# Kernel tuning notes

Hardware: AMD Instinct MI355X
Metric: run time of the kernel (lower is better)

Reference implementation:

```python
import jax, jax.numpy as jnp
import numpy as np

L = 2            # layer_num
NNEI = 120       # neighbors
ED = 64          # embed_dim
HD = 128         # hidden_dim
B = 4096         # nframes * nloc
SCALING = HD ** (-0.5)
LN_EPS = 1e-5


def _l2norm(x):
    # torch F.normalize: x / max(||x||, 1e-12)
    n = jnp.sqrt(jnp.sum(x * x, axis=-1, keepdims=True))
    return x / jnp.maximum(n, 1e-12)


def setup_inputs() -> dict:
    key = jax.random.key(0)
    ks = jax.random.split(key, 10)
    input_G = jax.random.normal(ks[0], (B, NNEI, ED), dtype=jnp.float32)
    nei_mask = jax.random.randint(ks[1], (B, NNEI), 0, 2) > 0
    nei_mask = nei_mask.at[:, 0].set(True)  # ensure >=1 valid neighbor (avoid all -inf rows)
    r = jax.random.normal(ks[2], (B, NNEI, 3), dtype=jnp.float32)
    input_r = _l2norm(r)  # normalized radial
    std_in = 1.0 / np.sqrt(3 * HD + ED)
    std_out = 1.0 / np.sqrt(ED + HD)
    in_w = jax.random.normal(ks[3], (L, ED, 3 * HD), dtype=jnp.float32) * std_in
    in_b = jax.random.normal(ks[4], (L, 3 * HD), dtype=jnp.float32)
    out_w = jax.random.normal(ks[5], (L, HD, ED), dtype=jnp.float32) * std_out
    out_b = jax.random.normal(ks[6], (L, ED), dtype=jnp.float32)
    ln_g = jnp.ones((L, ED), dtype=jnp.float32)
    ln_b = jnp.zeros((L, ED), dtype=jnp.float32)
    return {"input_G": input_G, "nei_mask": nei_mask, "input_r": input_r,
            "in_w": in_w, "in_b": in_b, "out_w": out_w, "out_b": out_b,
            "ln_g": ln_g, "ln_b": ln_b}


def _layer_norm(x, g, b):
    mu = jnp.mean(x, axis=-1, keepdims=True)
    var = jnp.mean((x - mu) ** 2, axis=-1, keepdims=True)
    return (x - mu) * jax.lax.rsqrt(var + LN_EPS) * g + b


def reference(input_G, nei_mask, input_r, in_w, in_b, out_w, out_b, ln_g, ln_b):
    # angular gate: [B, nnei, nnei]
    ang = jnp.einsum('bnd,bmd->bnm', input_r, input_r)
    mask_k = nei_mask[:, None, :]   # mask over keys
    mask_q = nei_mask[:, :, None]   # mask over queries
    x = input_G
    for l in range(L):
        residual = x
        qkv = jnp.einsum('bne,ef->bnf', x, in_w[l]) + in_b[l]
        q, k, v = jnp.split(qkv, 3, axis=-1)           # each [B, nnei, HD]
        q = _l2norm(q) * SCALING
        k = _l2norm(k)
        v = _l2norm(v)
        aw = jnp.einsum('bnh,bmh->bnm', q, k)
        aw = jnp.where(mask_k, aw, -jnp.inf)
        aw = jax.nn.softmax(aw, axis=-1)
        aw = jnp.where(mask_q, aw, 0.0)
        aw = aw * ang                                   # dotr angular gating
        o = jnp.einsum('bnm,bmh->bnh', aw, v)
        x = residual + jnp.einsum('bnh,he->bne', o, out_w[l]) + out_b[l]
        x = _layer_norm(x, ln_g[l], ln_b[l])            # post_ln
    return x
```

## Files before the change

kernel.cpp:

```cpp
#include <hip/hip_runtime.h>
#include <math.h>

#define LAYERS 2
#define NNEI 120
#define NPAD 128
#define ED 64
#define HD 128
#define NB 4096
#define F3 (3*HD)
#define SCALING 0.088388347648318447f
#define LN_EPS 1e-5f
#define T 1024
#define XP 72
#define QPAD 136

typedef unsigned short u16;
typedef unsigned int u32;
typedef unsigned char u8;
typedef float f32x4 __attribute__((ext_vector_type(4)));
typedef short bf16x8 __attribute__((ext_vector_type(8)));

__device__ __forceinline__ float bf2f(u16 u) { return __uint_as_float(((u32)u) << 16); }
__device__ __forceinline__ u16 f2bf(float f) {
  __bf16 b = (__bf16)f;
  return __builtin_bit_cast(u16, b);
}
__device__ __forceinline__ u32 pk2bf(float lo, float hi) {
  return (u32)f2bf(lo) | ((u32)f2bf(hi) << 16);
}
__device__ __forceinline__ float gldr(const void* p, long i, bool f32) {
  return f32 ? ((const float*)p)[i] : bf2f(((const u16*)p)[i]);
}
__device__ __forceinline__ float red16sum(float v) {
  v += __shfl_xor(v, 1); v += __shfl_xor(v, 2);
  v += __shfl_xor(v, 4); v += __shfl_xor(v, 8);
  return v;
}

#define MFMA(a, b, d) (d) = __builtin_amdgcn_mfma_f32_16x16x32_bf16((a), (b), (d), 0, 0, 0)

__device__ __forceinline__ void gload_lds16(const u16* src, u16* dst) {
  __builtin_amdgcn_global_load_lds(
      (const __attribute__((address_space(1))) u32*)(const void*)src,
      (__attribute__((address_space(3))) u32*)(void*)dst, 16, 0, 0);
}

__device__ __forceinline__ void stage16(const u16* __restrict__ hi, const u16* __restrict__ lo,
                                        long base, int kstride, u16* sbuf, int wave, int lane) {
  const int col = 4 * wave + (lane >> 4);
  const int slot = lane & 15;
  const int chunk = (slot & 7) ^ (col & 7);
  const u16* src = ((slot < 8) ? hi : lo) + base + (long)col * kstride + 8 * chunk;
  gload_lds16(src, sbuf + wave * 512);
}

__device__ __forceinline__ bf16x8 rdfrag(const u16* sbuf, int col, int chunk, int c7, int lo) {
  const int slot = (chunk ^ c7) + (lo << 3);
  return *(const bf16x8*)(sbuf + col * 128 + slot * 8);
}

__global__ void detect_kernel(const u16* __restrict__ G,
                              const u8* __restrict__ mask,
                              int* __restrict__ flags) {
  __shared__ int sf[2];
  const int t = threadIdx.x;
  if (t < 2) sf[t] = 0;
  __syncthreads();
  int isf = 0;
  for (int i = t; i < 256; i += 256) {
    int e = (G[2 * i] >> 7) & 0xff;
    if (e >= 150) isf = 1;
  }
  int mb = 0;
  for (int i = t; i < 4096; i += 256) {
    if (i && (i & 3) && mask[i]) mb = 1;
  }
  if (isf) atomicOr(&sf[0], 1);
  if (mb) atomicOr(&sf[1], 1);
  __syncthreads();
  if (t < 2) flags[t] = sf[t];
}

__global__ void prep_kernel(const void* __restrict__ in_w, const void* __restrict__ out_w,
                            u16* __restrict__ wt_hi, u16* __restrict__ wt_lo,
                            u16* __restrict__ ow_hi, u16* __restrict__ ow_lo,
                            const int* __restrict__ flags) {
  const bool f32 = flags[0] != 0;
  const int i = blockIdx.x * blockDim.x + threadIdx.x;
  if (i < LAYERS * F3 * ED) {
    const int l = i / (F3 * ED);
    const int rem = i % (F3 * ED);
    const int f = rem / ED;
    const int e = rem % ED;
    const long src = (long)(l * ED + e) * F3 + f;
    const float w = f32 ? ((const float*)in_w)[src] : bf2f(((const u16*)in_w)[src]);
    const u16 h = f2bf(w);
    wt_hi[i] = h;
    wt_lo[i] = f2bf(w - bf2f(h));
  }
  if (i < LAYERS * ED * HD) {
    const int l = i / (ED * HD);
    const int rem = i % (ED * HD);
    const int e = rem / HD;
    const int hh = rem % HD;
    const long src = (long)(l * HD + hh) * ED + e;
    const float w = f32 ? ((const float*)out_w)[src] : bf2f(((const u16*)out_w)[src]);
    const u16 h = f2bf(w);
    ow_hi[i] = h;
    ow_lo[i] = f2bf(w - bf2f(h));
  }
}

__global__ __launch_bounds__(T) void nwa_kernel(
    const void* __restrict__ G, const void* __restrict__ mask,
    const void* __restrict__ rr,
    const void* __restrict__ in_b, const void* __restrict__ out_b,
    const void* __restrict__ ln_g, const void* __restrict__ ln_b,
    const u16* __restrict__ wt_hi, const u16* __restrict__ wt_lo,
    const u16* __restrict__ ow_hi, const u16* __restrict__ ow_lo,
    void* __restrict__ out, const int* __restrict__ flags)
{
  const bool f32f = flags[0] != 0;
  const bool mbyte = flags[1] != 0;

  __shared__ __align__(16) u16 x_hi[NPAD][XP];
  __shared__ __align__(16) u16 x_lo[NPAD][XP];
  __shared__ __align__(16) u16 q_s[NPAD][QPAD];
  __shared__ __align__(16) u16 k_s[NPAD][QPAD];
  __shared__ __align__(16) u16 vT_s[HD][QPAD];
  __shared__ __align__(16) float r_s[NPAD][4];
  __shared__ __align__(16) float pA[2][8][16];
  __shared__ __align__(16) float pB[2][8][16];
  __shared__ int m_s[NPAD];

  const int b = blockIdx.x;
  const int t = threadIdx.x;
  const int wave = t >> 6;
  const int band = wave & 7;
  const int half = wave >> 3;
  const int lane = t & 63;
  const int g = lane >> 4;
  const int c = lane & 15;
  const int c7 = c & 7;
  u16* sbase = &q_s[0][0];

  {
    const long gbase = (long)b * (NNEI * ED);
    for (int i = t; i < NNEI * ED; i += T) {
      const int rrow = i >> 6, cc = i & 63;
      if (f32f) {
        const float v = ((const float*)G)[gbase + i];
        const u16 h = f2bf(v);
        x_hi[rrow][cc] = h;
        x_lo[rrow][cc] = f2bf(v - bf2f(h));
      } else {
        x_hi[rrow][cc] = ((const u16*)G)[gbase + i];
        x_lo[rrow][cc] = 0;
      }
    }
    for (int i = t; i < (NPAD - NNEI) * ED; i += T) {
      x_hi[NNEI + (i >> 6)][i & 63] = 0;
      x_lo[NNEI + (i >> 6)][i & 63] = 0;
    }
    const long rbase = (long)b * (NNEI * 3);
    const long mbase = (long)b * NNEI;
    for (int i = t; i < NPAD; i += T) {
      if (i < NNEI) {
        r_s[i][0] = gldr(rr, rbase + i * 3 + 0, f32f);
        r_s[i][1] = gldr(rr, rbase + i * 3 + 1, f32f);
        r_s[i][2] = gldr(rr, rbase + i * 3 + 2, f32f);
        r_s[i][3] = 0.f;
        m_s[i] = mbyte ? (int)((const u8*)mask)[mbase + i] : ((const int*)mask)[mbase + i];
      } else {
        r_s[i][0] = 0.f; r_s[i][1] = 0.f; r_s[i][2] = 0.f; r_s[i][3] = 0.f;
        m_s[i] = 0;
      }
    }
  }
  stage16(wt_hi, wt_lo, (long)2 * 4096, 64, sbase, wave, lane);
  __syncthreads();

  int vm[4];
  #pragma unroll
  for (int mtl = 0; mtl < 4; ++mtl) vm[mtl] = m_s[16 * (4 * half + mtl) + c];
  float qmr[4];
  #pragma unroll
  for (int r = 0; r < 4; ++r) qmr[r] = m_s[16 * band + 4 * g + r] ? 1.f : 0.f;

  for (int l = 0; l < LAYERS; ++l) {
    const long wofs = (long)l * (F3 * ED);
    const long bbase = (long)l * F3;
    const long oofs = (long)l * (ED * HD);
    const bool use_lo = f32f || (l > 0);

    bf16x8 a_hi[2], a_lo[2];
    #pragma unroll
    for (int kf = 0; kf < 2; ++kf) {
      a_hi[kf] = *(const bf16x8*)&x_hi[16 * band + c][32 * kf + 8 * g];
      a_lo[kf] = *(const bf16x8*)&x_lo[16 * band + c][32 * kf + 8 * g];
    }
    f32x4 accQ[4], accB[4];
    #pragma unroll
    for (int j = 0; j < 4; ++j) { accQ[j] = (f32x4){0,0,0,0}; accB[j] = (f32x4){0,0,0,0}; }

    #pragma unroll
    for (int ss = 0; ss < 6; ++ss) {
      const int n = (ss + 2) % 6;
      if (ss < 5)
        stage16(wt_hi, wt_lo, wofs + (long)((ss + 3) % 6) * 4096, 64,
                sbase + ((ss + 1) & 1) * 8192, wave, lane);
      if (ss == 2) {
        const f32x4 sa = *(const f32x4*)&pA[0][band][4 * g];
        const f32x4 sb4 = *(const f32x4*)&pA[1][band][4 * g];
        float invr[4];
        #pragma unroll
        for (int r = 0; r < 4; ++r) invr[r] = rsqrtf(fmaxf(sa[r] + sb4[r], 1e-24f));
        #pragma unroll
        for (int j = 0; j < 4; ++j) {
          const int nt = 4 * (j >> 1) + 2 * half + (j & 1);
          #pragma unroll
          for (int r = 0; r < 4; ++r)
            k_s[16 * band + 4 * g + r][16 * nt + c] = f2bf(accB[j][r] * invr[r]);
          accB[j] = (f32x4){0,0,0,0};
        }
      }
      if (ss == 4) {
        const f32x4 sa = *(const f32x4*)&pB[0][band][4 * g];
        const f32x4 sb4 = *(const f32x4*)&pB[1][band][4 * g];
        float invr[4];
        #pragma unroll
        for (int r = 0; r < 4; ++r) invr[r] = rsqrtf(fmaxf(sa[r] + sb4[r], 1e-24f));
        #pragma unroll
        for (int j = 0; j < 4; ++j) {
          const int nt = 4 * (j >> 1) + 2 * half + (j & 1);
          const u32 p01 = pk2bf(accB[j][0] * invr[0], accB[j][1] * invr[1]);
          const u32 p23 = pk2bf(accB[j][2] * invr[2], accB[j][3] * invr[3]);
          *(u32*)&vT_s[16 * nt + c][16 * band + 4 * g + 0] = p01;
          *(u32*)&vT_s[16 * nt + c][16 * band + 4 * g + 2] = p23;
        }
      }
      const u16* sb = sbase + (ss & 1) * 8192;
      #pragma unroll
      for (int ctl = 0; ctl < 2; ++ctl) {
        const int col = 16 * (2 * half + ctl) + c;
        const int j = 2 * (n & 1) + ctl;
        const bf16x8 bh0 = rdfrag(sb, col, g, c7, 0);
        const bf16x8 bh1 = rdfrag(sb, col, 4 + g, c7, 0);
        const bf16x8 bl0 = rdfrag(sb, col, g, c7, 1);
        const bf16x8 bl1 = rdfrag(sb, col, 4 + g, c7, 1);
        f32x4 d = (n < 2) ? accQ[j] : accB[j];
        MFMA(a_hi[0], bh0, d); MFMA(a_hi[1], bh1, d);
        if (use_lo) { MFMA(a_lo[0], bh0, d); MFMA(a_lo[1], bh1, d); }
        MFMA(a_hi[0], bl0, d); MFMA(a_hi[1], bl1, d);
        if (n < 2) accQ[j] = d; else accB[j] = d;
      }
      if (ss == 1 || ss == 3 || ss == 5) {
        const int fo = (ss == 1) ? 128 : (ss == 3) ? 256 : 0;
        f32x4* acc = (ss == 5) ? accQ : accB;
        #pragma unroll
        for (int j = 0; j < 4; ++j) {
          const int nt = 4 * (j >> 1) + 2 * half + (j & 1);
          const float bias = gldr(in_b, bbase + fo + 16 * nt + c, f32f);
          acc[j][0] += bias; acc[j][1] += bias; acc[j][2] += bias; acc[j][3] += bias;
        }
        float* dst = (ss == 3) ? &pB[half][band][0] : &pA[half][band][0];
        #pragma unroll
        for (int r = 0; r < 4; ++r) {
          const float ssum = acc[0][r] * acc[0][r] + acc[1][r] * acc[1][r] +
                             acc[2][r] * acc[2][r] + acc[3][r] * acc[3][r];
          const float red = red16sum(ssum);
          if (c == 0) dst[4 * g + r] = red;
        }
      }
      __syncthreads();
    }
    {
      const f32x4 sa = *(const f32x4*)&pA[0][band][4 * g];
      const f32x4 sb4 = *(const f32x4*)&pA[1][band][4 * g];
      float invr[4];
      #pragma unroll
      for (int r = 0; r < 4; ++r) invr[r] = SCALING * rsqrtf(fmaxf(sa[r] + sb4[r], 1e-24f));
      #pragma unroll
      for (int j = 0; j < 4; ++j) {
        const int nt = 4 * (j >> 1) + 2 * half + (j & 1);
        #pragma unroll
        for (int r = 0; r < 4; ++r)
          q_s[16 * band + 4 * g + r][16 * nt + c] = f2bf(accQ[j][r] * invr[r]);
      }
    }
    __syncthreads();

    f32x4 s4[4];
    {
      bf16x8 aq[4];
      #pragma unroll
      for (int kf = 0; kf < 4; ++kf)
        aq[kf] = *(const bf16x8*)&q_s[16 * band + c][32 * kf + 8 * g];
      #pragma unroll
      for (int mtl = 0; mtl < 4; ++mtl) {
        const u16* kp = &k_s[16 * (4 * half + mtl) + c][8 * g];
        f32x4 d = {0.f, 0.f, 0.f, 0.f};
        #pragma unroll
        for (int kf = 0; kf < 4; ++kf)
          MFMA(aq[kf], *(const bf16x8*)(kp + 32 * kf), d);
        s4[mtl] = d;
      }
    }
    {
      float psum[4] = {0.f, 0.f, 0.f, 0.f};
      #pragma unroll
      for (int mtl = 0; mtl < 4; ++mtl) {
        #pragma unroll
        for (int r = 0; r < 4; ++r) {
          const float e = vm[mtl] ? __expf(s4[mtl][r]) : 0.f;
          s4[mtl][r] = e;
          psum[r] += e;
        }
      }
      #pragma unroll
      for (int r = 0; r < 4; ++r) {
        const float red = red16sum(psum[r]);
        if (c == 0) pA[half][band][4 * g + r] = red;
      }
    }
    __syncthreads();
    {
      const f32x4 sa = *(const f32x4*)&pA[0][band][4 * g];
      const f32x4 sb4 = *(const f32x4*)&pA[1][band][4 * g];
      float inv[4];
      f32x4 rn[4];
      #pragma unroll
      for (int r = 0; r < 4; ++r) {
        inv[r] = qmr[r] / (sa[r] + sb4[r]);
        rn[r] = *(const f32x4*)&r_s[16 * band + 4 * g + r][0];
      }
      #pragma unroll
      for (int mtl = 0; mtl < 4; ++mtl) {
        const int mt = 4 * half + mtl;
        const f32x4 rm = *(const f32x4*)&r_s[16 * mt + c][0];
        #pragma unroll
        for (int r = 0; r < 4; ++r) {
          const float w = s4[mtl][r] * inv[r] *
              (rn[r][0] * rm[0] + rn[r][1] * rm[1] + rn[r][2] * rm[2]);
          q_s[16 * band + 4 * g + r][16 * mt + c] = f2bf(w);
        }
      }
    }
    __syncthreads();

    {
      bf16x8 pa[4];
      #pragma unroll
      for (int kf = 0; kf < 4; ++kf)
        pa[kf] = *(const bf16x8*)&q_s[16 * band + c][32 * kf + 8 * g];
      f32x4 o4[4];
      #pragma unroll
      for (int htl = 0; htl < 4; ++htl) {
        const u16* vp = &vT_s[16 * (4 * half + htl) + c][8 * g];
        f32x4 d = {0.f, 0.f, 0.f, 0.f};
        #pragma unroll
        for (int kf = 0; kf < 4; ++kf)
          MFMA(pa[kf], *(const bf16x8*)(vp + 32 * kf), d);
        o4[htl] = d;
      }
      #pragma unroll
      for (int htl = 0; htl < 4; ++htl)
        #pragma unroll
        for (int r = 0; r < 4; ++r)
          k_s[16 * band + 4 * g + r][16 * (4 * half + htl) + c] = f2bf(o4[htl][r]);
    }
    __syncthreads();

    bf16x8 ao[4];
    #pragma unroll
    for (int kf = 0; kf < 4; ++kf)
      ao[kf] = *(const bf16x8*)&k_s[16 * band + c][32 * kf + 8 * g];
    stage16(ow_hi, ow_lo, oofs, 128, sbase, wave, lane);
    __syncthreads();
    f32x4 dv[2];
    dv[0] = (f32x4){0,0,0,0}; dv[1] = (f32x4){0,0,0,0};
    #pragma unroll
    for (int kh = 0; kh < 2; ++kh) {
      if (kh == 0) stage16(ow_hi, ow_lo, oofs + 64, 128, sbase + 8192, wave, lane);
      const u16* sb = sbase + kh * 8192;
      #pragma unroll
      for (int ntl = 0; ntl < 2; ++ntl) {
        const int col = 16 * (2 * half + ntl) + c;
        #pragma unroll
        for (int kfl = 0; kfl < 2; ++kfl) {
          const bf16x8 bh = rdfrag(sb, col, 4 * kfl + g, c7, 0);
          const bf16x8 bl = rdfrag(sb, col, 4 * kfl + g, c7, 1);
          MFMA(ao[2 * kh + kfl], bh, dv[ntl]);
          MFMA(ao[2 * kh + kfl], bl, dv[ntl]);
        }
      }
      if (kh == 0) __syncthreads();
    }
    if (l + 1 < LAYERS)
      stage16(wt_hi, wt_lo, (long)(l + 1) * (F3 * ED) + (long)2 * 4096, 64, sbase, wave, lane);
    {
      #pragma unroll
      for (int ntl = 0; ntl < 2; ++ntl) {
        const int e0 = 16 * (2 * half + ntl) + c;
        const float ob = gldr(out_b, (long)l * ED + e0, f32f);
        #pragma unroll
        for (int r = 0; r < 4; ++r) {
          const int nrow = 16 * band + 4 * g + r;
          dv[ntl][r] += ob + bf2f(x_hi[nrow][e0]) + bf2f(x_lo[nrow][e0]);
        }
      }
      #pragma unroll
      for (int r = 0; r < 4; ++r) {
        const float sx = red16sum(dv[0][r] + dv[1][r]);
        const float sxx = red16sum(dv[0][r] * dv[0][r] + dv[1][r] * dv[1][r]);
        if (c == 0) { pA[half][band][4 * g + r] = sx; pB[half][band][4 * g + r] = sxx; }
      }
    }
    __syncthreads();
    {
      const f32x4 xa = *(const f32x4*)&pA[0][band][4 * g];
      const f32x4 xb = *(const f32x4*)&pA[1][band][4 * g];
      const f32x4 ya = *(const f32x4*)&pB[0][band][4 * g];
      const f32x4 yb = *(const f32x4*)&pB[1][band][4 * g];
      float gg[2], bbv[2];
      #pragma unroll
      for (int ntl = 0; ntl < 2; ++ntl) {
        const int e0 = 16 * (2 * half + ntl) + c;
        gg[ntl]  = gldr(ln_g, (long)l * ED + e0, f32f);
        bbv[ntl] = gldr(ln_b, (long)l * ED + e0, f32f);
      }
      #pragma unroll
      for (int r = 0; r < 4; ++r) {
        const int nrow = 16 * band + 4 * g + r;
        const float mu = (xa[r] + xb[r]) * (1.f / 64.f);
        const float ex2 = (ya[r] + yb[r]) * (1.f / 64.f);
        const float rs = rsqrtf(fmaxf(ex2 - mu * mu, 0.f) + LN_EPS);
        if (nrow < NNEI) {
          #pragma unroll
          for (int ntl = 0; ntl < 2; ++ntl) {
            const int e0 = 16 * (2 * half + ntl) + c;
            const float y = (dv[ntl][r] - mu) * rs * gg[ntl] + bbv[ntl];
            if (l + 1 < LAYERS) {
              const u16 hh2 = f2bf(y);
              x_hi[nrow][e0] = hh2;
              x_lo[nrow][e0] = f2bf(y - bf2f(hh2));
            } else {
              const long oidx = (long)b * (NNEI * ED) + (long)nrow * ED + e0;
              if (f32f) ((float*)out)[oidx] = y;
              else      ((u16*)out)[oidx] = f2bf(y);
            }
          }
        }
      }
    }
    if (l + 1 < LAYERS) __syncthreads();
  }
}

extern "C" void kernel_launch(void* const* d_in, const int* in_sizes, int n_in,
                              void* d_out, int out_size, void* d_ws, size_t ws_size,
                              hipStream_t stream) {
  (void)in_sizes; (void)n_in; (void)out_size; (void)ws_size;
  const void* G = d_in[0];
  const void* mask = d_in[1];
  const void* rr = d_in[2];
  const void* in_w = d_in[3];
  const void* in_b = d_in[4];
  const void* out_w = d_in[5];
  const void* out_b = d_in[6];
  const void* ln_g = d_in[7];
  const void* ln_b = d_in[8];

  int* flags = (int*)d_ws;
  u16* wt_hi = (u16*)((char*)d_ws + 256);
  u16* wt_lo = wt_hi + LAYERS * F3 * ED;
  u16* ow_hi = wt_lo + LAYERS * F3 * ED;
  u16* ow_lo = ow_hi + LAYERS * ED * HD;

  detect_kernel<<<dim3(1), dim3(256), 0, stream>>>((const u16*)G, (const u8*)mask, flags);
  prep_kernel<<<dim3(96), dim3(512), 0, stream>>>(in_w, out_w, wt_hi, wt_lo, ow_hi, ow_lo, flags);
  nwa_kernel<<<dim3(NB), dim3(T), 0, stream>>>(
      G, mask, rr, in_b, out_b, ln_g, ln_b, wt_hi, wt_lo, ow_hi, ow_lo, d_out, flags);
}
```

Before: 847.0 us.

## Drop weight lo-split, fp32 residual in LDS, triple-buffered staging with fine barriers

Weights are now stored only as bf16 hi parts, which removes the lo-weight MFMAs and halves the weight staging traffic. The activation x is kept in fp32 LDS and split into hi/lo in registers. Staging moves to a 3-slot ring with explicit vmcnt waits and lgkmcnt barriers, and the out_w prefetch is folded into the QKV loop. Q scaling is fused into the softmax exponent, LDS tiles use an XOR swizzle instead of padding, and bias and LN parameter loads are hoisted. Dropping the weight lo terms lowers accuracy relative to the fp32 reference.

Result: slower. 1.482 ms (+75.0%).

```diff
diff --git a/kernel.cpp b/kernel.cpp
--- a/kernel.cpp
+++ b/kernel.cpp
@@ -11,8 +11,7 @@
 #define SCALING 0.088388347648318447f
 #define LN_EPS 1e-5f
 #define T 1024
-#define XP 72
-#define QPAD 136
+#define XP 68
 
 typedef unsigned short u16;
 typedef unsigned int u32;
@@ -38,6 +37,9 @@
 }
 
 #define MFMA(a, b, d) (d) = __builtin_amdgcn_mfma_f32_16x16x32_bf16((a), (b), (d), 0, 0, 0)
+#define WVM(n) asm volatile("s_waitcnt vmcnt(" #n ")" ::: "memory")
+#define LBAR() do { asm volatile("s_waitcnt lgkmcnt(0)" ::: "memory"); \
+                    __builtin_amdgcn_s_barrier(); } while (0)
 
 __device__ __forceinline__ void gload_lds16(const u16* src, u16* dst) {
   __builtin_amdgcn_global_load_lds(
@@ -45,18 +47,21 @@
       (__attribute__((address_space(3))) u32*)(void*)dst, 16, 0, 0);
 }
 
-__device__ __forceinline__ void stage16(const u16* __restrict__ hi, const u16* __restrict__ lo,
-                                        long base, int kstride, u16* sbuf, int wave, int lane) {
-  const int col = 4 * wave + (lane >> 4);
-  const int slot = lane & 15;
-  const int chunk = (slot & 7) ^ (col & 7);
-  const u16* src = ((slot < 8) ? hi : lo) + base + (long)col * kstride + 8 * chunk;
-  gload_lds16(src, sbuf + wave * 512);
-}
-
-__device__ __forceinline__ bf16x8 rdfrag(const u16* sbuf, int col, int chunk, int c7, int lo) {
-  const int slot = (chunk ^ c7) + (lo << 3);
-  return *(const bf16x8*)(sbuf + col * 128 + slot * 8);
+__device__ __forceinline__ int swz(int row, int col) {
+  return (row << 7) + ((((col >> 3) ^ row) & 7) << 3) + (col & 7);
+}
+
+__device__ __forceinline__ void stage8k(const u16* __restrict__ src_base, long base,
+                                        int kstride, u16* sbuf, int wave, int lane) {
+  if (wave < 8) {
+    const int col = 8 * wave + (lane >> 3);
+    const int s = lane & 7;
+    const u16* src = src_base + base + (long)col * kstride + 8 * (s ^ (col & 7));
+    gload_lds16(src, sbuf + wave * 512);
+  }
+}
+__device__ __forceinline__ bf16x8 rdfrag(const u16* sbuf, int col, int kchunk) {
+  return *(const bf16x8*)(sbuf + col * 64 + 8 * (kchunk ^ (col & 7)));
 }
 
 __global__ void detect_kernel(const u16* __restrict__ G,
@@ -82,8 +87,7 @@
 }
 
 __global__ void prep_kernel(const void* __restrict__ in_w, const void* __restrict__ out_w,
-                            u16* __restrict__ wt_hi, u16* __restrict__ wt_lo,
-                            u16* __restrict__ ow_hi, u16* __restrict__ ow_lo,
+                            u16* __restrict__ wt_hi, u16* __restrict__ ow_hi,
                             const int* __restrict__ flags) {
   const bool f32 = flags[0] != 0;
   const int i = blockIdx.x * blockDim.x + threadIdx.x;
@@ -94,9 +98,7 @@
     const int e = rem % ED;
     const long src = (long)(l * ED + e) * F3 + f;
     const float w = f32 ? ((const float*)in_w)[src] : bf2f(((const u16*)in_w)[src]);
-    const u16 h = f2bf(w);
-    wt_hi[i] = h;
-    wt_lo[i] = f2bf(w - bf2f(h));
+    wt_hi[i] = f2bf(w);
   }
   if (i < LAYERS * ED * HD) {
     const int l = i / (ED * HD);
@@ -105,9 +107,7 @@
     const int hh = rem % HD;
     const long src = (long)(l * HD + hh) * ED + e;
     const float w = f32 ? ((const float*)out_w)[src] : bf2f(((const u16*)out_w)[src]);
-    const u16 h = f2bf(w);
-    ow_hi[i] = h;
-    ow_lo[i] = f2bf(w - bf2f(h));
+    ow_hi[i] = f2bf(w);
   }
 }
 
@@ -116,18 +116,17 @@
     const void* __restrict__ rr,
     const void* __restrict__ in_b, const void* __restrict__ out_b,
     const void* __restrict__ ln_g, const void* __restrict__ ln_b,
-    const u16* __restrict__ wt_hi, const u16* __restrict__ wt_lo,
-    const u16* __restrict__ ow_hi, const u16* __restrict__ ow_lo,
+    const u16* __restrict__ wt_hi, const u16* __restrict__ ow_hi,
     void* __restrict__ out, const int* __restrict__ flags)
 {
   const bool f32f = flags[0] != 0;
   const bool mbyte = flags[1] != 0;
 
-  __shared__ __align__(16) u16 x_hi[NPAD][XP];
-  __shared__ __align__(16) u16 x_lo[NPAD][XP];
-  __shared__ __align__(16) u16 q_s[NPAD][QPAD];
-  __shared__ __align__(16) u16 k_s[NPAD][QPAD];
-  __shared__ __align__(16) u16 vT_s[HD][QPAD];
+  __shared__ __align__(16) float x_s[NPAD][XP];
+  __shared__ __align__(16) u16 q_s[NPAD * 128];
+  __shared__ __align__(16) u16 k_s[NPAD * 128];
+  __shared__ __align__(16) u16 vT_s[NPAD * 128];
+  __shared__ __align__(16) u16 stg[3 * 4096];
   __shared__ __align__(16) float r_s[NPAD][4];
   __shared__ __align__(16) float pA[2][8][16];
   __shared__ __align__(16) float pB[2][8][16];
@@ -141,27 +140,13 @@
   const int lane = t & 63;
   const int g = lane >> 4;
   const int c = lane & 15;
-  const int c7 = c & 7;
-  u16* sbase = &q_s[0][0];
 
   {
     const long gbase = (long)b * (NNEI * ED);
-    for (int i = t; i < NNEI * ED; i += T) {
-      const int rrow = i >> 6, cc = i & 63;
-      if (f32f) {
-        const float v = ((const float*)G)[gbase + i];
-        const u16 h = f2bf(v);
-        x_hi[rrow][cc] = h;
-        x_lo[rrow][cc] = f2bf(v - bf2f(h));
-      } else {
-        x_hi[rrow][cc] = ((const u16*)G)[gbase + i];
-        x_lo[rrow][cc] = 0;
-      }
-    }
-    for (int i = t; i < (NPAD - NNEI) * ED; i += T) {
-      x_hi[NNEI + (i >> 6)][i & 63] = 0;
-      x_lo[NNEI + (i >> 6)][i & 63] = 0;
-    }
+    for (int i = t; i < NNEI * ED; i += T)
+      x_s[i >> 6][i & 63] = gldr(G, gbase + i, f32f);
+    for (int i = t; i < (NPAD - NNEI) * ED; i += T)
+      x_s[NNEI + (i >> 6)][i & 63] = 0.f;
     const long rbase = (long)b * (NNEI * 3);
     const long mbase = (long)b * NNEI;
     for (int i = t; i < NPAD; i += T) {
@@ -177,12 +162,12 @@
       }
     }
   }
-  stage16(wt_hi, wt_lo, (long)2 * 4096, 64, sbase, wave, lane);
+  stage8k(wt_hi, (long)2 * 4096, 64, stg, wave, lane);
   __syncthreads();
 
-  int vm[4];
+  int vm4 = 0;
   #pragma unroll
-  for (int mtl = 0; mtl < 4; ++mtl) vm[mtl] = m_s[16 * (4 * half + mtl) + c];
+  for (int mtl = 0; mtl < 4; ++mtl) vm4 |= (m_s[16 * (4 * half + mtl) + c] ? 1 : 0) << mtl;
   float qmr[4];
   #pragma unroll
   for (int r = 0; r < 4; ++r) qmr[r] = m_s[16 * band + 4 * g + r] ? 1.f : 0.f;
@@ -191,13 +176,46 @@
     const long wofs = (long)l * (F3 * ED);
     const long bbase = (long)l * F3;
     const long oofs = (long)l * (ED * HD);
+    const int base = l ? 2 : 0;
     const bool use_lo = f32f || (l > 0);
+
+    float bQv[4], bKv[4], bVv[4];
+    #pragma unroll
+    for (int j = 0; j < 4; ++j) {
+      const int nt = 4 * (j >> 1) + 2 * half + (j & 1);
+      bQv[j] = gldr(in_b, bbase + 16 * nt + c, f32f);
+      bKv[j] = gldr(in_b, bbase + 128 + 16 * nt + c, f32f);
+      bVv[j] = gldr(in_b, bbase + 256 + 16 * nt + c, f32f);
+    }
+    float obv[2], ggv[2], bbv[2];
+    #pragma unroll
+    for (int ntl = 0; ntl < 2; ++ntl) {
+      const int e0 = 16 * (2 * half + ntl) + c;
+      obv[ntl] = gldr(out_b, (long)l * ED + e0, f32f);
+      ggv[ntl] = gldr(ln_g, (long)l * ED + e0, f32f);
+      bbv[ntl] = gldr(ln_b, (long)l * ED + e0, f32f);
+    }
 
     bf16x8 a_hi[2], a_lo[2];
     #pragma unroll
     for (int kf = 0; kf < 2; ++kf) {
-      a_hi[kf] = *(const bf16x8*)&x_hi[16 * band + c][32 * kf + 8 * g];
-      a_lo[kf] = *(const bf16x8*)&x_lo[16 * band + c][32 * kf + 8 * g];
+      const float* xp = &x_s[16 * band + c][32 * kf + 8 * g];
+      const f32x4 xa = *(const f32x4*)xp;
+      const f32x4 xb = *(const f32x4*)(xp + 4);
+      float xf[8] = {xa[0], xa[1], xa[2], xa[3], xb[0], xb[1], xb[2], xb[3]};
+      #pragma unroll
+      for (int j2 = 0; j2 < 8; ++j2) {
+        const u16 h = f2bf(xf[j2]);
+        a_hi[kf][j2] = (short)h;
+        a_lo[kf][j2] = (short)0;
+      }
+      if (use_lo) {
+        #pragma unroll
+        for (int j2 = 0; j2 < 8; ++j2) {
+          const u16 h = f2bf(xf[j2]);
+          a_lo[kf][j2] = (short)f2bf(xf[j2] - bf2f(h));
+        }
+      }
     }
     f32x4 accQ[4], accB[4];
     #pragma unroll
@@ -206,9 +224,17 @@
     #pragma unroll
     for (int ss = 0; ss < 6; ++ss) {
       const int n = (ss + 2) % 6;
-      if (ss < 5)
-        stage16(wt_hi, wt_lo, wofs + (long)((ss + 3) % 6) * 4096, 64,
-                sbase + ((ss + 1) & 1) * 8192, wave, lane);
+      if (ss < 5) {
+        stage8k(wt_hi, wofs + (long)((ss + 3) % 6) * 4096, 64,
+                stg + ((base + ss + 1) % 3) * 4096, wave, lane);
+        WVM(1);
+      } else {
+        stage8k(ow_hi, oofs, 128, stg + ((base + 6) % 3) * 4096, wave, lane);
+        stage8k(ow_hi, oofs + 64, 128, stg + ((base + 7) % 3) * 4096, wave, lane);
+        WVM(2);
+      }
+      LBAR();
+
       if (ss == 2) {
         const f32x4 sa = *(const f32x4*)&pA[0][band][4 * g];
         const f32x4 sb4 = *(const f32x4*)&pA[1][band][4 * g];
@@ -220,7 +246,7 @@
           const int nt = 4 * (j >> 1) + 2 * half + (j & 1);
           #pragma unroll
           for (int r = 0; r < 4; ++r)
-            k_s[16 * band + 4 * g + r][16 * nt + c] = f2bf(accB[j][r] * invr[r]);
+            k_s[swz(16 * band + 4 * g + r, 16 * nt + c)] = f2bf(accB[j][r] * invr[r]);
           accB[j] = (f32x4){0,0,0,0};
         }
       }
@@ -235,84 +261,98 @@
           const int nt = 4 * (j >> 1) + 2 * half + (j & 1);
           const u32 p01 = pk2bf(accB[j][0] * invr[0], accB[j][1] * invr[1]);
           const u32 p23 = pk2bf(accB[j][2] * invr[2], accB[j][3] * invr[3]);
-          *(u32*)&vT_s[16 * nt + c][16 * band + 4 * g + 0] = p01;
-          *(u32*)&vT_s[16 * nt + c][16 * band + 4 * g + 2] = p23;
-        }
-      }
-      const u16* sb = sbase + (ss & 1) * 8192;
-      #pragma unroll
-      for (int ctl = 0; ctl < 2; ++ctl) {
-        const int col = 16 * (2 * half + ctl) + c;
-        const int j = 2 * (n & 1) + ctl;
-        const bf16x8 bh0 = rdfrag(sb, col, g, c7, 0);
-        const bf16x8 bh1 = rdfrag(sb, col, 4 + g, c7, 0);
-        const bf16x8 bl0 = rdfrag(sb, col, g, c7, 1);
-        const bf16x8 bl1 = rdfrag(sb, col, 4 + g, c7, 1);
-        f32x4 d = (n < 2) ? accQ[j] : accB[j];
-        MFMA(a_hi[0], bh0, d); MFMA(a_hi[1], bh1, d);
-        if (use_lo) { MFMA(a_lo[0], bh0, d); MFMA(a_lo[1], bh1, d); }
-        MFMA(a_hi[0], bl0, d); MFMA(a_hi[1], bl1, d);
-        if (n < 2) accQ[j] = d; else accB[j] = d;
-      }
-      if (ss == 1 || ss == 3 || ss == 5) {
-        const int fo = (ss == 1) ? 128 : (ss == 3) ? 256 : 0;
-        f32x4* acc = (ss == 5) ? accQ : accB;
+          const int o0 = swz(16 * nt + c, 16 * band + 4 * g);
+          *(u32*)&vT_s[o0] = p01;
+          *(u32*)&vT_s[o0 + 2] = p23;
+        }
+      }
+
+      {
+        const u16* sb = stg + ((base + ss) % 3) * 4096;
+        #pragma unroll
+        for (int ctl = 0; ctl < 2; ++ctl) {
+          const int col = 16 * (2 * half + ctl) + c;
+          const int j = 2 * (n & 1) + ctl;
+          const bf16x8 bh0 = rdfrag(sb, col, g);
+          const bf16x8 bh1 = rdfrag(sb, col, 4 + g);
+          f32x4 d = (n < 2) ? accQ[j] : accB[j];
+          MFMA(a_hi[0], bh0, d); MFMA(a_hi[1], bh1, d);
+          if (use_lo) { MFMA(a_lo[0], bh0, d); MFMA(a_lo[1], bh1, d); }
+          if (n < 2) accQ[j] = d; else accB[j] = d;
+        }
+      }
+
+      if (ss == 1 || ss == 3) {
+        const float* bv = (ss == 1) ? bKv : bVv;
+        #pragma unroll
+        for (int j = 0; j < 4; ++j) {
+          accB[j][0] += bv[j]; accB[j][1] += bv[j];
+          accB[j][2] += bv[j]; accB[j][3] += bv[j];
+        }
+        float* dst = (ss == 1) ? &pA[half][band][0] : &pB[half][band][0];
+        #pragma unroll
+        for (int r = 0; r < 4; ++r) {
+          const float ssum = accB[0][r] * accB[0][r] + accB[1][r] * accB[1][r] +
+                             accB[2][r] * accB[2][r] + accB[3][r] * accB[3][r];
+          const float red = red16sum(ssum);
+          if (c == 0) dst[4 * g + r] = red;
+        }
+      }
+      if (ss == 5) {
+        #pragma unroll
+        for (int j = 0; j < 4; ++j) {
+          accQ[j][0] += bQv[j]; accQ[j][1] += bQv[j];
+          accQ[j][2] += bQv[j]; accQ[j][3] += bQv[j];
+        }
+        #pragma unroll
+        for (int r = 0; r < 4; ++r) {
+          const float ssum = accQ[0][r] * accQ[0][r] + accQ[1][r] * accQ[1][r] +
+                             accQ[2][r] * accQ[2][r] + accQ[3][r] * accQ[3][r];
+          const float red = red16sum(ssum);
+          if (c == 0) pA[half][band][4 * g + r] = red;
+        }
         #pragma unroll
         for (int j = 0; j < 4; ++j) {
           const int nt = 4 * (j >> 1) + 2 * half + (j & 1);
-          const float bias = gldr(in_b, bbase + fo + 16 * nt + c, f32f);
-          acc[j][0] += bias; acc[j][1] += bias; acc[j][2] += bias; acc[j][3] += bias;
-        }
-        float* dst = (ss == 3) ? &pB[half][band][0] : &pA[half][band][0];
+          #pragma unroll
+          for (int r = 0; r < 4; ++r)
+            q_s[swz(16 * band + 4 * g + r, 16 * nt + c)] = f2bf(accQ[j][r]);
+        }
+      }
+    }
+    LBAR();
+
+    float invq[4];
+    {
+      const f32x4 qa = *(const f32x4*)&pA[0][band][4 * g];
+      const f32x4 qb = *(const f32x4*)&pA[1][band][4 * g];
+      #pragma unroll
+      for (int r = 0; r < 4; ++r)
+        invq[r] = SCALING * rsqrtf(fmaxf(qa[r] + qb[r], 1e-24f));
+    }
+    f32x4 s4[4];
+    {
+      bf16x8 aq[4];
+      #pragma unroll
+      for (int kf = 0; kf < 4; ++kf)
+        aq[kf] = *(const bf16x8*)&q_s[swz(16 * band + c, 8 * g + 32 * kf)];
+      #pragma unroll
+      for (int mtl = 0; mtl < 4; ++mtl) {
+        f32x4 d = {0.f, 0.f, 0.f, 0.f};
+        #pragma unroll
+        for (int kf = 0; kf < 4; ++kf)
+          MFMA(aq[kf], *(const bf16x8*)&k_s[swz(16 * (4 * half + mtl) + c, 8 * g + 32 * kf)], d);
+        s4[mtl] = d;
+      }
+    }
+    {
+      float psum[4] = {0.f, 0.f, 0.f, 0.f};
+      #pragma unroll
+      for (int mtl = 0; mtl < 4; ++mtl) {
+        const float vmf = ((vm4 >> mtl) & 1) ? 1.f : 0.f;
         #pragma unroll
         for (int r = 0; r < 4; ++r) {
-          const float ssum = acc[0][r] * acc[0][r] + acc[1][r] * acc[1][r] +
-                             acc[2][r] * acc[2][r] + acc[3][r] * acc[3][r];
-          const float red = red16sum(ssum);
-          if (c == 0) dst[4 * g + r] = red;
-        }
-      }
-      __syncthreads();
-    }
-    {
-      const f32x4 sa = *(const f32x4*)&pA[0][band][4 * g];
-      const f32x4 sb4 = *(const f32x4*)&pA[1][band][4 * g];
-      float invr[4];
-      #pragma unroll
-      for (int r = 0; r < 4; ++r) invr[r] = SCALING * rsqrtf(fmaxf(sa[r] + sb4[r], 1e-24f));
-      #pragma unroll
-      for (int j = 0; j < 4; ++j) {
-        const int nt = 4 * (j >> 1) + 2 * half + (j & 1);
-        #pragma unroll
-        for (int r = 0; r < 4; ++r)
-          q_s[16 * band + 4 * g + r][16 * nt + c] = f2bf(accQ[j][r] * invr[r]);
-      }
-    }
-    __syncthreads();
-
-    f32x4 s4[4];
-    {
-      bf16x8 aq[4];
-      #pragma unroll
-      for (int kf = 0; kf < 4; ++kf)
-        aq[kf] = *(const bf16x8*)&q_s[16 * band + c][32 * kf + 8 * g];
-      #pragma unroll
-      for (int mtl = 0; mtl < 4; ++mtl) {
-        const u16* kp = &k_s[16 * (4 * half + mtl) + c][8 * g];
-        f32x4 d = {0.f, 0.f, 0.f, 0.f};
-        #pragma unroll
-        for (int kf = 0; kf < 4; ++kf)
-          MFMA(aq[kf], *(const bf16x8*)(kp + 32 * kf), d);
-        s4[mtl] = d;
-      }
-    }
-    {
-      float psum[4] = {0.f, 0.f, 0.f, 0.f};
-      #pragma unroll
-      for (int mtl = 0; mtl < 4; ++mtl) {
-        #pragma unroll
-        for (int r = 0; r < 4; ++r) {
-          const float e = vm[mtl] ? __expf(s4[mtl][r]) : 0.f;
+          const float e = vmf * __expf(s4[mtl][r] * invq[r]);
           s4[mtl][r] = e;
           psum[r] += e;
         }
@@ -320,13 +360,13 @@
       #pragma unroll
       for (int r = 0; r < 4; ++r) {
         const float red = red16sum(psum[r]);
-        if (c == 0) pA[half][band][4 * g + r] = red;
-      }
-    }
-    __syncthreads();
-    {
-      const f32x4 sa = *(const f32x4*)&pA[0][band][4 * g];
-      const f32x4 sb4 = *(const f32x4*)&pA[1][band][4 * g];
+        if (c == 0) pB[half][band][4 * g + r] = red;
+      }
+    }
+    LBAR();
+    {
+      const f32x4 sa = *(const f32x4*)&pB[0][band][4 * g];
+      const f32x4 sb4 = *(const f32x4*)&pB[1][band][4 * g];
       float inv[4];
       f32x4 rn[4];
       #pragma unroll
@@ -342,72 +382,60 @@
         for (int r = 0; r < 4; ++r) {
           const float w = s4[mtl][r] * inv[r] *
               (rn[r][0] * rm[0] + rn[r][1] * rm[1] + rn[r][2] * rm[2]);
-          q_s[16 * band + 4 * g + r][16 * mt + c] = f2bf(w);
-        }
-      }
-    }
-    __syncthreads();
+          k_s[swz(16 * band + 4 * g + r, 16 * mt + c)] = f2bf(w);
+        }
+      }
+    }
+    LBAR();
 
     {
       bf16x8 pa[4];
       #pragma unroll
       for (int kf = 0; kf < 4; ++kf)
-        pa[kf] = *(const bf16x8*)&q_s[16 * band + c][32 * kf + 8 * g];
-      f32x4 o4[4];
+        pa[kf] = *(const bf16x8*)&k_s[swz(16 * band + c, 8 * g + 32 * kf)];
       #pragma unroll
       for (int htl = 0; htl < 4; ++htl) {
-        const u16* vp = &vT_s[16 * (4 * half + htl) + c][8 * g];
         f32x4 d = {0.f, 0.f, 0.f, 0.f};
         #pragma unroll
         for (int kf = 0; kf < 4; ++kf)
-          MFMA(pa[kf], *(const bf16x8*)(vp + 32 * kf), d);
-        o4[htl] = d;
-      }
-      #pragma unroll
-      for (int htl = 0; htl < 4; ++htl)
+          MFMA(pa[kf], *(const bf16x8*)&vT_s[swz(16 * (4 * half + htl) + c, 8 * g + 32 * kf)], d);
         #pragma unroll
         for (int r = 0; r < 4; ++r)
-          k_s[16 * band + 4 * g + r][16 * (4 * half + htl) + c] = f2bf(o4[htl][r]);
-    }
-    __syncthreads();
-
-    bf16x8 ao[4];
-    #pragma unroll
-    for (int kf = 0; kf < 4; ++kf)
-      ao[kf] = *(const bf16x8*)&k_s[16 * band + c][32 * kf + 8 * g];
-    stage16(ow_hi, ow_lo, oofs, 128, sbase, wave, lane);
-    __syncthreads();
+          q_s[swz(16 * band + 4 * g + r, 16 * (4 * half + htl) + c)] = f2bf(d[r]);
+      }
+    }
+    WVM(0);
+    LBAR();
+
     f32x4 dv[2];
     dv[0] = (f32x4){0,0,0,0}; dv[1] = (f32x4){0,0,0,0};
-    #pragma unroll
-    for (int kh = 0; kh < 2; ++kh) {
-      if (kh == 0) stage16(ow_hi, ow_lo, oofs + 64, 128, sbase + 8192, wave, lane);
-      const u16* sb = sbase + kh * 8192;
-      #pragma unroll
-      for (int ntl = 0; ntl < 2; ++ntl) {
-        const int col = 16 * (2 * half + ntl) + c;
-        #pragma unroll
-        for (int kfl = 0; kfl < 2; ++kfl) {
-          const bf16x8 bh = rdfrag(sb, col, 4 * kfl + g, c7, 0);
-          const bf16x8 bl = rdfrag(sb, col, 4 * kfl + g, c7, 1);
-          MFMA(ao[2 * kh + kfl], bh, dv[ntl]);
-          MFMA(ao[2 * kh + kfl], bl, dv[ntl]);
-        }
-      }
-      if (kh == 0) __syncthreads();
+    {
+      bf16x8 ao[4];
+      #pragma unroll
+      for (int kf = 0; kf < 4; ++kf)
+        ao[kf] = *(const bf16x8*)&q_s[swz(16 * band + c, 8 * g + 32 * kf)];
+      #pragma unroll
+      for (int kh = 0; kh < 2; ++kh) {
+        const u16* sb = stg + ((base + 6 + kh) % 3) * 4096;
+        #pragma unroll
+        for (int ntl = 0; ntl < 2; ++ntl) {
+          const int col = 16 * (2 * half + ntl) + c;
+          #pragma unroll
+          for (int kfl = 0; kfl < 2; ++kfl)
+            MFMA(ao[2 * kh + kfl], rdfrag(sb, col, 4 * kfl + g), dv[ntl]);
+        }
+      }
     }
     if (l + 1 < LAYERS)
-      stage16(wt_hi, wt_lo, (long)(l + 1) * (F3 * ED) + (long)2 * 4096, 64, sbase, wave, lane);
+      stage8k(wt_hi, (long)(l + 1) * (F3 * ED) + (long)2 * 4096, 64,
+              stg + ((base + 8) % 3) * 4096, wave, lane);
     {
       #pragma unroll
       for (int ntl = 0; ntl < 2; ++ntl) {
         const int e0 = 16 * (2 * half + ntl) + c;
-        const float ob = gldr(out_b, (long)l * ED + e0, f32f);
-        #pragma unroll
-        for (int r = 0; r < 4; ++r) {
-          const int nrow = 16 * band + 4 * g + r;
-          dv[ntl][r] += ob + bf2f(x_hi[nrow][e0]) + bf2f(x_lo[nrow][e0]);
-        }
+        #pragma unroll
+        for (int r = 0; r < 4; ++r)
+          dv[ntl][r] += obv[ntl] + x_s[16 * band + 4 * g + r][e0];
       }
       #pragma unroll
       for (int r = 0; r < 4; ++r) {
@@ -416,19 +444,12 @@
         if (c == 0) { pA[half][band][4 * g + r] = sx; pB[half][band][4 * g + r] = sxx; }
       }
     }
-    __syncthreads();
+    LBAR();
     {
       const f32x4 xa = *(const f32x4*)&pA[0][band][4 * g];
       const f32x4 xb = *(const f32x4*)&pA[1][band][4 * g];
       const f32x4 ya = *(const f32x4*)&pB[0][band][4 * g];
       const f32x4 yb = *(const f32x4*)&pB[1][band][4 * g];
-      float gg[2], bbv[2];
-      #pragma unroll
-      for (int ntl = 0; ntl < 2; ++ntl) {
-        const int e0 = 16 * (2 * half + ntl) + c;
-        gg[ntl]  = gldr(ln_g, (long)l * ED + e0, f32f);
-        bbv[ntl] = gldr(ln_b, (long)l * ED + e0, f32f);
-      }
       #pragma unroll
       for (int r = 0; r < 4; ++r) {
         const int nrow = 16 * band + 4 * g + r;
@@ -439,11 +460,9 @@
           #pragma unroll
           for (int ntl = 0; ntl < 2; ++ntl) {
             const int e0 = 16 * (2 * half + ntl) + c;
-            const float y = (dv[ntl][r] - mu) * rs * gg[ntl] + bbv[ntl];
+            const float y = (dv[ntl][r] - mu) * rs * ggv[ntl] + bbv[ntl];
             if (l + 1 < LAYERS) {
-              const u16 hh2 = f2bf(y);
-              x_hi[nrow][e0] = hh2;
-              x_lo[nrow][e0] = f2bf(y - bf2f(hh2));
+              x_s[nrow][e0] = y;
             } else {
               const long oidx = (long)b * (NNEI * ED) + (long)nrow * ED + e0;
               if (f32f) ((float*)out)[oidx] = y;
@@ -453,7 +472,7 @@
         }
       }
     }
-    if (l + 1 < LAYERS) __syncthreads();
+    if (l + 1 < LAYERS) LBAR();
   }
 }
 
@@ -473,12 +492,10 @@
 
   int* flags = (int*)d_ws;
   u16* wt_hi = (u16*)((char*)d_ws + 256);
-  u16* wt_lo = wt_hi + LAYERS * F3 * ED;
-  u16* ow_hi = wt_lo + LAYERS * F3 * ED;
-  u16* ow_lo = ow_hi + LAYERS * ED * HD;
+  u16* ow_hi = wt_hi + LAYERS * F3 * ED;
 
   detect_kernel<<<dim3(1), dim3(256), 0, stream>>>((const u16*)G, (const u8*)mask, flags);
-  prep_kernel<<<dim3(96), dim3(512), 0, stream>>>(in_w, out_w, wt_hi, wt_lo, ow_hi, ow_lo, flags);
+  prep_kernel<<<dim3(96), dim3(512), 0, stream>>>(in_w, out_w, wt_hi, ow_hi, flags);
   nwa_kernel<<<dim3(NB), dim3(T), 0, stream>>>(
-      G, mask, rr, in_b, out_b, ln_g, ln_b, wt_hi, wt_lo, ow_hi, ow_lo, d_out, flags);
-}
+      G, mask, rr, in_b, out_b, ln_g, ln_b, wt_hi, ow_hi, d_out, flags);
+}
```
